# Optimization experiments

Measured on AMD Instinct MI355X. Metric: run time of the kernel, lower is better.

The kernel has to match this reference:

```python
import jax, jax.numpy as jnp
import numpy as np

B, T, H = 1024, 1024, 64


def _lstm_cell(x, h, c, w_ih, w_hh, b_ih, b_hh):
    # gates: [B, 4H] in PyTorch order i, f, g, o
    g = x @ w_ih.T + h @ w_hh.T + b_ih + b_hh
    i, f, gg, o = jnp.split(g, 4, axis=-1)
    i = jax.nn.sigmoid(i)
    f = jax.nn.sigmoid(f)
    gg = jnp.tanh(gg)
    o = jax.nn.sigmoid(o)
    c_new = f * c + i * gg
    h_new = o * jnp.tanh(c_new)
    return h_new, c_new


def setup_inputs() -> dict:
    key = jax.random.key(0)
    ks = jax.random.split(key, 12)
    s = 1.0 / np.sqrt(H)  # torch default init scale
    r = lambda k, shape: jax.random.normal(k, shape, dtype=jnp.float32) * s
    return {
        "x": jax.random.normal(ks[0], (B, T), dtype=jnp.float32),
        "w_ih1": r(ks[1], (4 * H, 1)),
        "w_hh1": r(ks[2], (4 * H, H)),
        "b_ih1": r(ks[3], (4 * H,)),
        "b_hh1": r(ks[4], (4 * H,)),
        "w_ih2": r(ks[5], (4 * H, H)),
        "w_hh2": r(ks[6], (4 * H, H)),
        "b_ih2": r(ks[7], (4 * H,)),
        "b_hh2": r(ks[8], (4 * H,)),
        "w_lin": r(ks[9], (1, H)),
        "b_lin": r(ks[10], (1,)),
        "future_preds": 0,
    }


def reference(x, w_ih1, w_hh1, b_ih1, b_hh1, w_ih2, w_hh2, b_ih2, b_hh2,
              w_lin, b_lin, future_preds):
    bsz = x.shape[0]
    h1 = jnp.zeros((bsz, H), x.dtype)
    c1 = jnp.zeros((bsz, H), x.dtype)
    h2 = jnp.zeros((bsz, H), x.dtype)
    c2 = jnp.zeros((bsz, H), x.dtype)

    def step(carry, x_t):
        h1, c1, h2, c2 = carry
        h1, c1 = _lstm_cell(x_t, h1, c1, w_ih1, w_hh1, b_ih1, b_hh1)
        h2, c2 = _lstm_cell(h1, h2, c2, w_ih2, w_hh2, b_ih2, b_hh2)
        out = h2 @ w_lin.T + b_lin  # [B, 1]
        return (h1, c1, h2, c2), out

    xs = x.T[:, :, None]  # [T, B, 1]
    carry, outs = jax.lax.scan(step, (h1, c1, h2, c2), xs)
    outputs = outs[:, :, 0].T  # [B, T]

    if future_preds > 0:
        last = outs[-1]  # [B, 1]

        def fstep(carry, _):
            h1, c1, h2, c2, prev = carry
            h1, c1 = _lstm_cell(prev, h1, c1, w_ih1, w_hh1, b_ih1, b_hh1)
            h2, c2 = _lstm_cell(h1, h2, c2, w_ih2, w_hh2, b_ih2, b_hh2)
            out = h2 @ w_lin.T + b_lin
            return (h1, c1, h2, c2, out), out

        _, fouts = jax.lax.scan(fstep, (*carry, last), None, length=future_preds)
        outputs = jnp.concatenate([outputs, fouts[:, :, 0].T], axis=1)

    return outputs
```

## Files before the change

### kernel.cpp

```cpp
#include <hip/hip_runtime.h>
#include <hip/hip_bf16.h>


typedef _Float16 f16x8 __attribute__((ext_vector_type(8)));
typedef float    f32x4 __attribute__((ext_vector_type(4)));

namespace {
constexpr int Bb = 1024;
constexpr int Tt = 1024;
constexpr int NBat = 4;
constexpr int HSTR = 80;
constexpr int XSTR = 1025;

__device__ __forceinline__ float sigm_pre(float a) {
    return __builtin_amdgcn_rcpf(1.0f + __builtin_amdgcn_exp2f(a));
}
__device__ __forceinline__ float tanh_pre(float a) {
    return fmaf(2.0f, __builtin_amdgcn_rcpf(1.0f + __builtin_amdgcn_exp2f(a)), -1.0f);
}
__device__ __forceinline__ float tanh_f(float x) {
    float e = __builtin_amdgcn_exp2f(-2.8853900817779268f * x);
    return fmaf(2.0f, __builtin_amdgcn_rcpf(1.0f + e), -1.0f);
}
__device__ __forceinline__ bool detect_f32(const void* w) {
    const unsigned short* p = (const unsigned short*)w;
    int sane = 0;
    for (int i = 0; i < 64; ++i) {
        int e = (p[2 * i] >> 7) & 0xFF;
        if (e >= 107 && e <= 129) ++sane;
    }
    return sane < 32;
}
__device__ __forceinline__ float ld(const void* p, int i, bool f32) {
    return f32 ? ((const float*)p)[i]
               : __bfloat162float(((const __hip_bfloat16*)p)[i]);
}
__device__ __forceinline__ void st(void* p, int i, float v, bool f32) {
    if (f32) ((float*)p)[i] = v;
    else     ((__hip_bfloat16*)p)[i] = __float2bfloat16(v);
}
__device__ __forceinline__ void poll_flags(const int* f, int tp, int tq, int lane) {
    const int idx = lane & 7;
    const int thr = (idx < 4) ? tp : tq;
    for (;;) {
        int v = ((const volatile int*)f)[idx];
        if (__all(v >= thr)) break;
    }
    __builtin_amdgcn_sched_barrier(0);
    asm volatile("" ::: "memory");
}
}

__global__ __launch_bounds__(512, 1) void lstm2_kernel(
    const void* __restrict__ x,
    const void* __restrict__ w_ih1,
    const void* __restrict__ w_hh1,
    const void* __restrict__ b_ih1,
    const void* __restrict__ b_hh1,
    const void* __restrict__ w_ih2,
    const void* __restrict__ w_hh2,
    const void* __restrict__ b_ih2,
    const void* __restrict__ b_hh2,
    const void* __restrict__ w_lin,
    const void* __restrict__ b_lin,
    void* __restrict__ out)
{
    const int tid  = threadIdx.x;
    const int lane = tid & 63;
    const int w    = tid >> 6;
    const int gw   = w & 3;
    const bool isP = w < 4;
    const int m    = lane & 15;
    const int quad = lane >> 4;
    const int bb   = blockIdx.x * NBat;

    const bool f32 = detect_f32(w_hh1);

    __shared__ float                  xs[NBat * XSTR];
    __shared__ __align__(16) _Float16 h1ring[4][NBat * HSTR];
    __shared__ __align__(16) _Float16 h2buf[2][NBat * HSTR];
    __shared__ __align__(16) float    headp[4][NBat][4];
    __shared__ float                  outbuf[NBat * Tt];
    __shared__ int                    flg[8];

    for (int i = tid; i < NBat * 1024; i += 512)
        xs[(i >> 10) * XSTR + (i & 1023)] = ld(x, (bb + (i >> 10)) * Tt + (i & 1023), f32);
    for (int i = tid; i < NBat * HSTR; i += 512) {
        h1ring[0][i] = (_Float16)0; h1ring[1][i] = (_Float16)0;
        h1ring[2][i] = (_Float16)0; h1ring[3][i] = (_Float16)0;
        h2buf[0][i] = (_Float16)0;  h2buf[1][i] = (_Float16)0;
    }
    if (tid < 8) flg[tid] = 0;

    const int arow = lane & 15;
    const int g_ld = arow & 3;
    const int u_ld = arow >> 2;
    const float scA = (g_ld == 2) ? -2.8853900817779268f : -1.4426950408889634f;
    f16x8 wfA[4][2], wfB[4][2];
    {
        const void* MA = isP ? w_hh1 : w_ih2;
#pragma unroll
        for (int q = 0; q < 4; ++q) {
            const int row = 64 * g_ld + 16 * gw + 4 * q + u_ld;
#pragma unroll
            for (int s = 0; s < 2; ++s) {
                const int base = row * 64 + 32 * s + quad * 8;
                if (f32) {
                    const float* A = (const float*)MA;
                    const float* B = (const float*)w_hh2;
#pragma unroll
                    for (int j = 0; j < 8; ++j) {
                        wfA[q][s][j] = (_Float16)(scA * A[base + j]);
                        wfB[q][s][j] = isP ? (_Float16)0.0f
                                           : (_Float16)(scA * B[base + j]);
                    }
                } else {
                    const __hip_bfloat16* A = (const __hip_bfloat16*)MA;
                    const __hip_bfloat16* B = (const __hip_bfloat16*)w_hh2;
#pragma unroll
                    for (int j = 0; j < 8; ++j) {
                        wfA[q][s][j] = (_Float16)(scA * __bfloat162float(A[base + j]));
                        wfB[q][s][j] = isP ? (_Float16)0.0f
                                           : (_Float16)(scA * __bfloat162float(B[base + j]));
                    }
                }
            }
        }
    }
    f32x4 bv[4], wxv[4];
#pragma unroll
    for (int q = 0; q < 4; ++q)
#pragma unroll
        for (int r = 0; r < 4; ++r) {
            const int row = 64 * r + 16 * gw + 4 * q + quad;
            const float sg = (r == 2) ? -2.8853900817779268f : -1.4426950408889634f;
            bv[q][r] = sg * (isP ? (ld(b_ih1, row, f32) + ld(b_hh1, row, f32))
                                 : (ld(b_ih2, row, f32) + ld(b_hh2, row, f32)));
            wxv[q][r] = isP ? sg * ld(w_ih1, row, f32) : 0.0f;
        }
    const int q2   = m >> 2;
    const int bsel = m & 3;
    const int hidx = bsel * HSTR + 16 * gw + 4 * q2 + quad;
    const bool s1 = (q2 & 1) != 0, s2 = (q2 & 2) != 0;
    const float wl_u = ld(w_lin, 16 * gw + 4 * q2 + quad, f32);
    const float blin = ld(b_lin, 0, f32);
    float cst = 0.0f;
    __syncthreads();

    if (isP) {
#pragma unroll 4
        for (int t = 0; t < Tt; ++t) {
            const float xt = xs[bsel * XSTR + t];
            f32x4 ai[4];
#pragma unroll
            for (int q = 0; q < 4; ++q)
#pragma unroll
                for (int r = 0; r < 4; ++r)
                    ai[q][r] = fmaf(xt, wxv[q][r], bv[q][r]);
            poll_flags(flg, t, t - 3, lane);
            f32x4 acc[4];
            if (t > 0) {
                const _Float16* hp = h1ring[(t - 1) & 3] + bsel * HSTR;
                const f16x8 pa0 = *(const f16x8*)(hp + quad * 8);
                const f16x8 pa1 = *(const f16x8*)(hp + 32 + quad * 8);
                __builtin_amdgcn_s_setprio(1);
#pragma unroll
                for (int q = 0; q < 4; ++q) {
                    f32x4 p0 = __builtin_amdgcn_mfma_f32_16x16x32_f16(wfA[q][0], pa0, ai[q], 0, 0, 0);
                    f32x4 p1 = __builtin_amdgcn_mfma_f32_16x16x32_f16(wfA[q][1], pa1, f32x4{0,0,0,0}, 0, 0, 0);
                    acc[q] = p0 + p1;
                }
                __builtin_amdgcn_s_setprio(0);
            } else {
#pragma unroll
                for (int q = 0; q < 4; ++q) acc[q] = ai[q];
            }
            f32x4 g;
#pragma unroll
            for (int r = 0; r < 4; ++r) {
                float lo = s1 ? acc[1][r] : acc[0][r];
                float hi = s1 ? acc[3][r] : acc[2][r];
                g[r] = s2 ? hi : lo;
            }
            float ig = sigm_pre(g[0]), fg = sigm_pre(g[1]);
            float gg = tanh_pre(g[2]), og = sigm_pre(g[3]);
            cst = fmaf(fg, cst, ig * gg);
            h1ring[t & 3][hidx] = (_Float16)(og * tanh_f(cst));
            if (lane == 0) {
                asm volatile("" ::: "memory");
                *(volatile int*)&flg[gw] = t + 1;
            }
        }
    } else {
#pragma unroll 4
        for (int u = 0; u < Tt; ++u) {
            poll_flags(flg, u + 1, u, lane);
            if (u > 1 && w == 4 && lane < NBat) {
                f32x4 v = *(const f32x4*)&headp[(u - 2) & 3][lane][0];
                outbuf[lane * Tt + (u - 2)] = blin + (v[0] + v[1]) + (v[2] + v[3]);
            }
            const _Float16* h1p = h1ring[u & 3] + bsel * HSTR;
            const _Float16* h2p = h2buf[(u + 1) & 1] + bsel * HSTR;
            const f16x8 pa0 = *(const f16x8*)(h1p + quad * 8);
            const f16x8 pa1 = *(const f16x8*)(h1p + 32 + quad * 8);
            const f16x8 pb0 = *(const f16x8*)(h2p + quad * 8);
            const f16x8 pb1 = *(const f16x8*)(h2p + 32 + quad * 8);
            f32x4 acc[4];
            __builtin_amdgcn_s_setprio(1);
#pragma unroll
            for (int q = 0; q < 4; ++q) {
                f32x4 p2 = __builtin_amdgcn_mfma_f32_16x16x32_f16(wfA[q][0], pa0, bv[q], 0, 0, 0);
                p2 = __builtin_amdgcn_mfma_f32_16x16x32_f16(wfA[q][1], pa1, p2, 0, 0, 0);
                f32x4 p3 = __builtin_amdgcn_mfma_f32_16x16x32_f16(wfB[q][0], pb0, f32x4{0,0,0,0}, 0, 0, 0);
                p3 = __builtin_amdgcn_mfma_f32_16x16x32_f16(wfB[q][1], pb1, p3, 0, 0, 0);
                acc[q] = p2 + p3;
            }
            __builtin_amdgcn_s_setprio(0);
            f32x4 g;
#pragma unroll
            for (int r = 0; r < 4; ++r) {
                float lo = s1 ? acc[1][r] : acc[0][r];
                float hi = s1 ? acc[3][r] : acc[2][r];
                g[r] = s2 ? hi : lo;
            }
            float ig = sigm_pre(g[0]), fg = sigm_pre(g[1]);
            float gg = tanh_pre(g[2]), og = sigm_pre(g[3]);
            cst = fmaf(fg, cst, ig * gg);
            float h = og * tanh_f(cst);
            h2buf[u & 1][hidx] = (_Float16)h;
            if (lane == 0) {
                asm volatile("" ::: "memory");
                *(volatile int*)&flg[4 + gw] = u + 1;
            }
            float p = h * wl_u;
            p += __shfl_xor(p, 4);
            p += __shfl_xor(p, 8);
            p += __shfl_xor(p, 16);
            p += __shfl_xor(p, 32);
            if (lane < NBat)
                headp[u & 3][lane][gw] = p;
        }
        if (w == 4) {
            poll_flags(flg, 0, Tt, lane);
            if (lane < NBat) {
                f32x4 v2 = *(const f32x4*)&headp[(Tt - 2) & 3][lane][0];
                outbuf[lane * Tt + (Tt - 2)] = blin + (v2[0] + v2[1]) + (v2[2] + v2[3]);
                f32x4 v1 = *(const f32x4*)&headp[(Tt - 1) & 3][lane][0];
                outbuf[lane * Tt + (Tt - 1)] = blin + (v1[0] + v1[1]) + (v1[2] + v1[3]);
            }
        }
    }
    __syncthreads();
    for (int i = tid; i < NBat * Tt; i += 512)
        st(out, (bb + (i >> 10)) * Tt + (i & 1023), outbuf[i], f32);
}

extern "C" void kernel_launch(void* const* d_in, const int* in_sizes, int n_in,
                              void* d_out, int out_size, void* d_ws, size_t ws_size,
                              hipStream_t stream)
{
    (void)in_sizes; (void)n_in; (void)out_size; (void)d_ws; (void)ws_size;
    lstm2_kernel<<<dim3(Bb / NBat), dim3(512), 0, stream>>>(
        d_in[0], d_in[1], d_in[2], d_in[3], d_in[4], d_in[5],
        d_in[6], d_in[7], d_in[8], d_in[9], d_in[10], d_out);
}
```

Measured before the change: 718.0 us.

## Split block batch into two interleaved groups to overlap recurrent step latency

Splits the four batch rows each block handles into two independent groups of two, each with its own h ring buffers, head partials and sync flags, and interleaves their timestep processing in both the layer-1 and layer-2 wavefronts. The aim is to hide the serial MFMA, activation and flag-poll latency of one group behind the work of the other. In exchange, each group's MFMA uses only 2 of 16 B columns, so half the lanes compute duplicate results that are not stored. It also doubles the number of MFMAs and flag polls per timestep.

Result: slower. 1.295 ms (+80.4%).

```diff
diff --git a/kernel.cpp b/kernel.cpp
--- a/kernel.cpp
+++ b/kernel.cpp
@@ -9,6 +9,8 @@
 constexpr int Bb = 1024;
 constexpr int Tt = 1024;
 constexpr int NBat = 4;
+constexpr int NG   = 2;
+constexpr int GB   = 2;
 constexpr int HSTR = 80;
 constexpr int XSTR = 1025;
 
@@ -77,20 +79,19 @@
     const bool f32 = detect_f32(w_hh1);
 
     __shared__ float                  xs[NBat * XSTR];
-    __shared__ __align__(16) _Float16 h1ring[4][NBat * HSTR];
-    __shared__ __align__(16) _Float16 h2buf[2][NBat * HSTR];
-    __shared__ __align__(16) float    headp[4][NBat][4];
+    __shared__ __align__(16) _Float16 h1ring[NG][4][GB * HSTR];
+    __shared__ __align__(16) _Float16 h2buf[NG][2][GB * HSTR];
+    __shared__ __align__(16) float    headp[NG][4][GB][4];
     __shared__ float                  outbuf[NBat * Tt];
-    __shared__ int                    flg[8];
+    __shared__ int                    flg[NG][8];
 
     for (int i = tid; i < NBat * 1024; i += 512)
         xs[(i >> 10) * XSTR + (i & 1023)] = ld(x, (bb + (i >> 10)) * Tt + (i & 1023), f32);
-    for (int i = tid; i < NBat * HSTR; i += 512) {
-        h1ring[0][i] = (_Float16)0; h1ring[1][i] = (_Float16)0;
-        h1ring[2][i] = (_Float16)0; h1ring[3][i] = (_Float16)0;
-        h2buf[0][i] = (_Float16)0;  h2buf[1][i] = (_Float16)0;
-    }
-    if (tid < 8) flg[tid] = 0;
+    for (int i = tid; i < NG * 4 * GB * HSTR; i += 512)
+        (&h1ring[0][0][0])[i] = (_Float16)0;
+    for (int i = tid; i < NG * 2 * GB * HSTR; i += 512)
+        (&h2buf[0][0][0])[i] = (_Float16)0;
+    if (tid < NG * 8) (&flg[0][0])[tid] = 0;
 
     const int arow = lane & 15;
     const int g_ld = arow & 3;
@@ -138,115 +139,127 @@
                                  : (ld(b_ih2, row, f32) + ld(b_hh2, row, f32)));
             wxv[q][r] = isP ? sg * ld(w_ih1, row, f32) : 0.0f;
         }
-    const int q2   = m >> 2;
-    const int bsel = m & 3;
+    const int bsel = m & 1;
+    const int q2   = (m >> 1) & 3;
+    const bool dup = (m & 8) != 0;
     const int hidx = bsel * HSTR + 16 * gw + 4 * q2 + quad;
-    const bool s1 = (q2 & 1) != 0, s2 = (q2 & 2) != 0;
+    const bool s1 = (m & 2) != 0, s2 = (m & 4) != 0;
     const float wl_u = ld(w_lin, 16 * gw + 4 * q2 + quad, f32);
     const float blin = ld(b_lin, 0, f32);
-    float cst = 0.0f;
+    float csA = 0.0f, csB = 0.0f;
     __syncthreads();
 
     if (isP) {
 #pragma unroll 4
         for (int t = 0; t < Tt; ++t) {
-            const float xt = xs[bsel * XSTR + t];
-            f32x4 ai[4];
-#pragma unroll
-            for (int q = 0; q < 4; ++q)
-#pragma unroll
-                for (int r = 0; r < 4; ++r)
-                    ai[q][r] = fmaf(xt, wxv[q][r], bv[q][r]);
-            poll_flags(flg, t, t - 3, lane);
-            f32x4 acc[4];
-            if (t > 0) {
-                const _Float16* hp = h1ring[(t - 1) & 3] + bsel * HSTR;
-                const f16x8 pa0 = *(const f16x8*)(hp + quad * 8);
-                const f16x8 pa1 = *(const f16x8*)(hp + 32 + quad * 8);
-                __builtin_amdgcn_s_setprio(1);
-#pragma unroll
-                for (int q = 0; q < 4; ++q) {
-                    f32x4 p0 = __builtin_amdgcn_mfma_f32_16x16x32_f16(wfA[q][0], pa0, ai[q], 0, 0, 0);
-                    f32x4 p1 = __builtin_amdgcn_mfma_f32_16x16x32_f16(wfA[q][1], pa1, f32x4{0,0,0,0}, 0, 0, 0);
-                    acc[q] = p0 + p1;
-                }
-                __builtin_amdgcn_s_setprio(0);
-            } else {
-#pragma unroll
-                for (int q = 0; q < 4; ++q) acc[q] = ai[q];
-            }
-            f32x4 g;
-#pragma unroll
-            for (int r = 0; r < 4; ++r) {
-                float lo = s1 ? acc[1][r] : acc[0][r];
-                float hi = s1 ? acc[3][r] : acc[2][r];
-                g[r] = s2 ? hi : lo;
-            }
-            float ig = sigm_pre(g[0]), fg = sigm_pre(g[1]);
-            float gg = tanh_pre(g[2]), og = sigm_pre(g[3]);
-            cst = fmaf(fg, cst, ig * gg);
-            h1ring[t & 3][hidx] = (_Float16)(og * tanh_f(cst));
-            if (lane == 0) {
-                asm volatile("" ::: "memory");
-                *(volatile int*)&flg[gw] = t + 1;
+#pragma unroll
+            for (int g = 0; g < NG; ++g) {
+                float& cs = (g == 0) ? csA : csB;
+                const float xt = xs[(g * GB + bsel) * XSTR + t];
+                f32x4 ai[4];
+#pragma unroll
+                for (int q = 0; q < 4; ++q)
+#pragma unroll
+                    for (int r = 0; r < 4; ++r)
+                        ai[q][r] = fmaf(xt, wxv[q][r], bv[q][r]);
+                poll_flags(&flg[g][0], t, t - 3, lane);
+                f32x4 acc[4];
+                if (t > 0) {
+                    const _Float16* hp = &h1ring[g][(t - 1) & 3][bsel * HSTR];
+                    const f16x8 pa0 = *(const f16x8*)(hp + quad * 8);
+                    const f16x8 pa1 = *(const f16x8*)(hp + 32 + quad * 8);
+                    __builtin_amdgcn_s_setprio(1);
+#pragma unroll
+                    for (int q = 0; q < 4; ++q) {
+                        f32x4 p0 = __builtin_amdgcn_mfma_f32_16x16x32_f16(wfA[q][0], pa0, ai[q], 0, 0, 0);
+                        f32x4 p1 = __builtin_amdgcn_mfma_f32_16x16x32_f16(wfA[q][1], pa1, f32x4{0,0,0,0}, 0, 0, 0);
+                        acc[q] = p0 + p1;
+                    }
+                    __builtin_amdgcn_s_setprio(0);
+                } else {
+#pragma unroll
+                    for (int q = 0; q < 4; ++q) acc[q] = ai[q];
+                }
+                f32x4 gt;
+#pragma unroll
+                for (int r = 0; r < 4; ++r) {
+                    float lo = s1 ? acc[1][r] : acc[0][r];
+                    float hi = s1 ? acc[3][r] : acc[2][r];
+                    gt[r] = s2 ? hi : lo;
+                }
+                float ig = sigm_pre(gt[0]), fg = sigm_pre(gt[1]);
+                float gg = tanh_pre(gt[2]), og = sigm_pre(gt[3]);
+                cs = fmaf(fg, cs, ig * gg);
+                float h = og * tanh_f(cs);
+                if (!dup) h1ring[g][t & 3][hidx] = (_Float16)h;
+                if (lane == 0) {
+                    asm volatile("" ::: "memory");
+                    *(volatile int*)&flg[g][gw] = t + 1;
+                }
             }
         }
     } else {
 #pragma unroll 4
         for (int u = 0; u < Tt; ++u) {
-            poll_flags(flg, u + 1, u, lane);
-            if (u > 1 && w == 4 && lane < NBat) {
-                f32x4 v = *(const f32x4*)&headp[(u - 2) & 3][lane][0];
-                outbuf[lane * Tt + (u - 2)] = blin + (v[0] + v[1]) + (v[2] + v[3]);
-            }
-            const _Float16* h1p = h1ring[u & 3] + bsel * HSTR;
-            const _Float16* h2p = h2buf[(u + 1) & 1] + bsel * HSTR;
-            const f16x8 pa0 = *(const f16x8*)(h1p + quad * 8);
-            const f16x8 pa1 = *(const f16x8*)(h1p + 32 + quad * 8);
-            const f16x8 pb0 = *(const f16x8*)(h2p + quad * 8);
-            const f16x8 pb1 = *(const f16x8*)(h2p + 32 + quad * 8);
-            f32x4 acc[4];
-            __builtin_amdgcn_s_setprio(1);
-#pragma unroll
-            for (int q = 0; q < 4; ++q) {
-                f32x4 p2 = __builtin_amdgcn_mfma_f32_16x16x32_f16(wfA[q][0], pa0, bv[q], 0, 0, 0);
-                p2 = __builtin_amdgcn_mfma_f32_16x16x32_f16(wfA[q][1], pa1, p2, 0, 0, 0);
-                f32x4 p3 = __builtin_amdgcn_mfma_f32_16x16x32_f16(wfB[q][0], pb0, f32x4{0,0,0,0}, 0, 0, 0);
-                p3 = __builtin_amdgcn_mfma_f32_16x16x32_f16(wfB[q][1], pb1, p3, 0, 0, 0);
-                acc[q] = p2 + p3;
-            }
-            __builtin_amdgcn_s_setprio(0);
-            f32x4 g;
-#pragma unroll
-            for (int r = 0; r < 4; ++r) {
-                float lo = s1 ? acc[1][r] : acc[0][r];
-                float hi = s1 ? acc[3][r] : acc[2][r];
-                g[r] = s2 ? hi : lo;
-            }
-            float ig = sigm_pre(g[0]), fg = sigm_pre(g[1]);
-            float gg = tanh_pre(g[2]), og = sigm_pre(g[3]);
-            cst = fmaf(fg, cst, ig * gg);
-            float h = og * tanh_f(cst);
-            h2buf[u & 1][hidx] = (_Float16)h;
-            if (lane == 0) {
-                asm volatile("" ::: "memory");
-                *(volatile int*)&flg[4 + gw] = u + 1;
-            }
-            float p = h * wl_u;
-            p += __shfl_xor(p, 4);
-            p += __shfl_xor(p, 8);
-            p += __shfl_xor(p, 16);
-            p += __shfl_xor(p, 32);
-            if (lane < NBat)
-                headp[u & 3][lane][gw] = p;
+#pragma unroll
+            for (int g = 0; g < NG; ++g) {
+                float& cs = (g == 0) ? csA : csB;
+                poll_flags(&flg[g][0], u + 1, u, lane);
+                if (u > 1 && w == 4 && lane < GB) {
+                    f32x4 v = *(const f32x4*)&headp[g][(u - 2) & 3][lane][0];
+                    outbuf[(g * GB + lane) * Tt + (u - 2)] = blin + (v[0] + v[1]) + (v[2] + v[3]);
+                }
+                const _Float16* h1p = &h1ring[g][u & 3][bsel * HSTR];
+                const _Float16* h2p = &h2buf[g][(u + 1) & 1][bsel * HSTR];
+                const f16x8 pa0 = *(const f16x8*)(h1p + quad * 8);
+                const f16x8 pa1 = *(const f16x8*)(h1p + 32 + quad * 8);
+                const f16x8 pb0 = *(const f16x8*)(h2p + quad * 8);
+                const f16x8 pb1 = *(const f16x8*)(h2p + 32 + quad * 8);
+                f32x4 acc[4];
+                __builtin_amdgcn_s_setprio(1);
+#pragma unroll
+                for (int q = 0; q < 4; ++q) {
+                    f32x4 p2 = __builtin_amdgcn_mfma_f32_16x16x32_f16(wfA[q][0], pa0, bv[q], 0, 0, 0);
+                    p2 = __builtin_amdgcn_mfma_f32_16x16x32_f16(wfA[q][1], pa1, p2, 0, 0, 0);
+                    f32x4 p3 = __builtin_amdgcn_mfma_f32_16x16x32_f16(wfB[q][0], pb0, f32x4{0,0,0,0}, 0, 0, 0);
+                    p3 = __builtin_amdgcn_mfma_f32_16x16x32_f16(wfB[q][1], pb1, p3, 0, 0, 0);
+                    acc[q] = p2 + p3;
+                }
+                __builtin_amdgcn_s_setprio(0);
+                f32x4 gt;
+#pragma unroll
+                for (int r = 0; r < 4; ++r) {
+                    float lo = s1 ? acc[1][r] : acc[0][r];
+                    float hi = s1 ? acc[3][r] : acc[2][r];
+                    gt[r] = s2 ? hi : lo;
+                }
+                float ig = sigm_pre(gt[0]), fg = sigm_pre(gt[1]);
+                float gg = tanh_pre(gt[2]), og = sigm_pre(gt[3]);
+                cs = fmaf(fg, cs, ig * gg);
+                float h = og * tanh_f(cs);
+                if (!dup) h2buf[g][u & 1][hidx] = (_Float16)h;
+                if (lane == 0) {
+                    asm volatile("" ::: "memory");
+                    *(volatile int*)&flg[g][4 + gw] = u + 1;
+                }
+                float p = h * wl_u;
+                p += __shfl_xor(p, 2);
+                p += __shfl_xor(p, 4);
+                p += __shfl_xor(p, 16);
+                p += __shfl_xor(p, 32);
+                if (lane < GB) headp[g][u & 3][lane][gw] = p;
+            }
         }
         if (w == 4) {
-            poll_flags(flg, 0, Tt, lane);
-            if (lane < NBat) {
-                f32x4 v2 = *(const f32x4*)&headp[(Tt - 2) & 3][lane][0];
-                outbuf[lane * Tt + (Tt - 2)] = blin + (v2[0] + v2[1]) + (v2[2] + v2[3]);
-                f32x4 v1 = *(const f32x4*)&headp[(Tt - 1) & 3][lane][0];
-                outbuf[lane * Tt + (Tt - 1)] = blin + (v1[0] + v1[1]) + (v1[2] + v1[3]);
+#pragma unroll
+            for (int g = 0; g < NG; ++g) {
+                poll_flags(&flg[g][0], 0, Tt, lane);
+                if (lane < GB) {
+                    f32x4 v2 = *(const f32x4*)&headp[g][(Tt - 2) & 3][lane][0];
+                    outbuf[(g * GB + lane) * Tt + (Tt - 2)] = blin + (v2[0] + v2[1]) + (v2[2] + v2[3]);
+                    f32x4 v1 = *(const f32x4*)&headp[g][(Tt - 1) & 3][lane][0];
+                    outbuf[(g * GB + lane) * Tt + (Tt - 1)] = blin + (v1[0] + v1[1]) + (v1[2] + v1[3]);
+                }
             }
         }
     }
```

## Merge layer-1 and layer-2 wavefronts into one skewed per-wave pipeline

Applied to the files above, without the earlier changes.

Replaces the producer/consumer split (4 waves for layer 1, 4 for layer 2, 512 threads) with 4 waves that each compute layer 1 at step t and layer 2 at step t-1, using 256 threads per block. Each wave now holds all three weight matrices in registers and only one set of flags is polled per step, with an epilogue for the final layer-2 step. This cuts cross-wave flag handshakes and wave count, at the cost of serializing both layers' MFMA and activation work within a wave and raising register pressure.

Result: slower. 1.038 ms (+44.6%).

```diff
diff --git a/kernel.cpp b/kernel.cpp
--- a/kernel.cpp
+++ b/kernel.cpp
@@ -39,9 +39,8 @@
     if (f32) ((float*)p)[i] = v;
     else     ((__hip_bfloat16*)p)[i] = __float2bfloat16(v);
 }
-__device__ __forceinline__ void poll_flags(const int* f, int tp, int tq, int lane) {
-    const int idx = lane & 7;
-    const int thr = (idx < 4) ? tp : tq;
+__device__ __forceinline__ void poll_flags(const int* f, int thr, int lane) {
+    const int idx = lane & 3;
     for (;;) {
         int v = ((const volatile int*)f)[idx];
         if (__all(v >= thr)) break;
@@ -51,7 +50,7 @@
 }
 }
 
-__global__ __launch_bounds__(512, 1) void lstm2_kernel(
+__global__ __launch_bounds__(256, 1) void lstm2_kernel(
     const void* __restrict__ x,
     const void* __restrict__ w_ih1,
     const void* __restrict__ w_hh1,
@@ -67,9 +66,7 @@
 {
     const int tid  = threadIdx.x;
     const int lane = tid & 63;
-    const int w    = tid >> 6;
-    const int gw   = w & 3;
-    const bool isP = w < 4;
+    const int gw   = tid >> 6;
     const int m    = lane & 15;
     const int quad = lane >> 4;
     const int bb   = blockIdx.x * NBat;
@@ -81,62 +78,61 @@
     __shared__ __align__(16) _Float16 h2buf[2][NBat * HSTR];
     __shared__ __align__(16) float    headp[4][NBat][4];
     __shared__ float                  outbuf[NBat * Tt];
-    __shared__ int                    flg[8];
-
-    for (int i = tid; i < NBat * 1024; i += 512)
+    __shared__ int                    flg[4];
+
+    for (int i = tid; i < NBat * 1024; i += 256)
         xs[(i >> 10) * XSTR + (i & 1023)] = ld(x, (bb + (i >> 10)) * Tt + (i & 1023), f32);
-    for (int i = tid; i < NBat * HSTR; i += 512) {
+    for (int i = tid; i < NBat * HSTR; i += 256) {
         h1ring[0][i] = (_Float16)0; h1ring[1][i] = (_Float16)0;
         h1ring[2][i] = (_Float16)0; h1ring[3][i] = (_Float16)0;
         h2buf[0][i] = (_Float16)0;  h2buf[1][i] = (_Float16)0;
     }
-    if (tid < 8) flg[tid] = 0;
+    if (tid < 4) flg[tid] = 0;
 
     const int arow = lane & 15;
     const int g_ld = arow & 3;
     const int u_ld = arow >> 2;
     const float scA = (g_ld == 2) ? -2.8853900817779268f : -1.4426950408889634f;
-    f16x8 wfA[4][2], wfB[4][2];
-    {
-        const void* MA = isP ? w_hh1 : w_ih2;
-#pragma unroll
-        for (int q = 0; q < 4; ++q) {
-            const int row = 64 * g_ld + 16 * gw + 4 * q + u_ld;
-#pragma unroll
-            for (int s = 0; s < 2; ++s) {
-                const int base = row * 64 + 32 * s + quad * 8;
-                if (f32) {
-                    const float* A = (const float*)MA;
-                    const float* B = (const float*)w_hh2;
-#pragma unroll
-                    for (int j = 0; j < 8; ++j) {
-                        wfA[q][s][j] = (_Float16)(scA * A[base + j]);
-                        wfB[q][s][j] = isP ? (_Float16)0.0f
-                                           : (_Float16)(scA * B[base + j]);
-                    }
-                } else {
-                    const __hip_bfloat16* A = (const __hip_bfloat16*)MA;
-                    const __hip_bfloat16* B = (const __hip_bfloat16*)w_hh2;
-#pragma unroll
-                    for (int j = 0; j < 8; ++j) {
-                        wfA[q][s][j] = (_Float16)(scA * __bfloat162float(A[base + j]));
-                        wfB[q][s][j] = isP ? (_Float16)0.0f
-                                           : (_Float16)(scA * __bfloat162float(B[base + j]));
-                    }
+    f16x8 wf1[4][2], wf2[4][2], wf3[4][2];
+#pragma unroll
+    for (int q = 0; q < 4; ++q) {
+        const int row = 64 * g_ld + 16 * gw + 4 * q + u_ld;
+#pragma unroll
+        for (int s = 0; s < 2; ++s) {
+            const int base = row * 64 + 32 * s + quad * 8;
+            if (f32) {
+                const float* A1 = (const float*)w_hh1;
+                const float* A2 = (const float*)w_ih2;
+                const float* A3 = (const float*)w_hh2;
+#pragma unroll
+                for (int j = 0; j < 8; ++j) {
+                    wf1[q][s][j] = (_Float16)(scA * A1[base + j]);
+                    wf2[q][s][j] = (_Float16)(scA * A2[base + j]);
+                    wf3[q][s][j] = (_Float16)(scA * A3[base + j]);
                 }
-            }
-        }
-    }
-    f32x4 bv[4], wxv[4];
+            } else {
+                const __hip_bfloat16* A1 = (const __hip_bfloat16*)w_hh1;
+                const __hip_bfloat16* A2 = (const __hip_bfloat16*)w_ih2;
+                const __hip_bfloat16* A3 = (const __hip_bfloat16*)w_hh2;
+#pragma unroll
+                for (int j = 0; j < 8; ++j) {
+                    wf1[q][s][j] = (_Float16)(scA * __bfloat162float(A1[base + j]));
+                    wf2[q][s][j] = (_Float16)(scA * __bfloat162float(A2[base + j]));
+                    wf3[q][s][j] = (_Float16)(scA * __bfloat162float(A3[base + j]));
+                }
+            }
+        }
+    }
+    f32x4 bv1[4], bv2[4], wxv[4];
 #pragma unroll
     for (int q = 0; q < 4; ++q)
 #pragma unroll
         for (int r = 0; r < 4; ++r) {
             const int row = 64 * r + 16 * gw + 4 * q + quad;
             const float sg = (r == 2) ? -2.8853900817779268f : -1.4426950408889634f;
-            bv[q][r] = sg * (isP ? (ld(b_ih1, row, f32) + ld(b_hh1, row, f32))
-                                 : (ld(b_ih2, row, f32) + ld(b_hh2, row, f32)));
-            wxv[q][r] = isP ? sg * ld(w_ih1, row, f32) : 0.0f;
+            bv1[q][r] = sg * (ld(b_ih1, row, f32) + ld(b_hh1, row, f32));
+            bv2[q][r] = sg * (ld(b_ih2, row, f32) + ld(b_hh2, row, f32));
+            wxv[q][r] = sg * ld(w_ih1, row, f32);
         }
     const int q2   = m >> 2;
     const int bsel = m & 3;
@@ -144,114 +140,147 @@
     const bool s1 = (q2 & 1) != 0, s2 = (q2 & 2) != 0;
     const float wl_u = ld(w_lin, 16 * gw + 4 * q2 + quad, f32);
     const float blin = ld(b_lin, 0, f32);
-    float cst = 0.0f;
+    float c1 = 0.0f, c2 = 0.0f;
+    f16x8 pa0{}, pa1{};
     __syncthreads();
 
-    if (isP) {
 #pragma unroll 4
-        for (int t = 0; t < Tt; ++t) {
-            const float xt = xs[bsel * XSTR + t];
-            f32x4 ai[4];
-#pragma unroll
-            for (int q = 0; q < 4; ++q)
-#pragma unroll
-                for (int r = 0; r < 4; ++r)
-                    ai[q][r] = fmaf(xt, wxv[q][r], bv[q][r]);
-            poll_flags(flg, t, t - 3, lane);
+    for (int t = 0; t < Tt; ++t) {
+        const float xt = xs[bsel * XSTR + t];
+        f32x4 ai[4];
+#pragma unroll
+        for (int q = 0; q < 4; ++q)
+#pragma unroll
+            for (int r = 0; r < 4; ++r)
+                ai[q][r] = fmaf(xt, wxv[q][r], bv1[q][r]);
+        poll_flags(flg, t, lane);
+        f32x4 g1;
+        if (t > 0) {
+            const _Float16* hp = h1ring[(t - 1) & 3] + bsel * HSTR;
+            pa0 = *(const f16x8*)(hp + quad * 8);
+            pa1 = *(const f16x8*)(hp + 32 + quad * 8);
             f32x4 acc[4];
-            if (t > 0) {
-                const _Float16* hp = h1ring[(t - 1) & 3] + bsel * HSTR;
-                const f16x8 pa0 = *(const f16x8*)(hp + quad * 8);
-                const f16x8 pa1 = *(const f16x8*)(hp + 32 + quad * 8);
-                __builtin_amdgcn_s_setprio(1);
-#pragma unroll
-                for (int q = 0; q < 4; ++q) {
-                    f32x4 p0 = __builtin_amdgcn_mfma_f32_16x16x32_f16(wfA[q][0], pa0, ai[q], 0, 0, 0);
-                    f32x4 p1 = __builtin_amdgcn_mfma_f32_16x16x32_f16(wfA[q][1], pa1, f32x4{0,0,0,0}, 0, 0, 0);
-                    acc[q] = p0 + p1;
-                }
-                __builtin_amdgcn_s_setprio(0);
-            } else {
-#pragma unroll
-                for (int q = 0; q < 4; ++q) acc[q] = ai[q];
-            }
-            f32x4 g;
+            __builtin_amdgcn_s_setprio(1);
+#pragma unroll
+            for (int q = 0; q < 4; ++q) {
+                f32x4 p0 = __builtin_amdgcn_mfma_f32_16x16x32_f16(wf1[q][0], pa0, ai[q], 0, 0, 0);
+                f32x4 p1 = __builtin_amdgcn_mfma_f32_16x16x32_f16(wf1[q][1], pa1, f32x4{0,0,0,0}, 0, 0, 0);
+                acc[q] = p0 + p1;
+            }
+            __builtin_amdgcn_s_setprio(0);
 #pragma unroll
             for (int r = 0; r < 4; ++r) {
                 float lo = s1 ? acc[1][r] : acc[0][r];
                 float hi = s1 ? acc[3][r] : acc[2][r];
-                g[r] = s2 ? hi : lo;
-            }
-            float ig = sigm_pre(g[0]), fg = sigm_pre(g[1]);
-            float gg = tanh_pre(g[2]), og = sigm_pre(g[3]);
-            cst = fmaf(fg, cst, ig * gg);
-            h1ring[t & 3][hidx] = (_Float16)(og * tanh_f(cst));
-            if (lane == 0) {
-                asm volatile("" ::: "memory");
-                *(volatile int*)&flg[gw] = t + 1;
-            }
-        }
-    } else {
-#pragma unroll 4
-        for (int u = 0; u < Tt; ++u) {
-            poll_flags(flg, u + 1, u, lane);
-            if (u > 1 && w == 4 && lane < NBat) {
-                f32x4 v = *(const f32x4*)&headp[(u - 2) & 3][lane][0];
-                outbuf[lane * Tt + (u - 2)] = blin + (v[0] + v[1]) + (v[2] + v[3]);
-            }
-            const _Float16* h1p = h1ring[u & 3] + bsel * HSTR;
-            const _Float16* h2p = h2buf[(u + 1) & 1] + bsel * HSTR;
-            const f16x8 pa0 = *(const f16x8*)(h1p + quad * 8);
-            const f16x8 pa1 = *(const f16x8*)(h1p + 32 + quad * 8);
+                g1[r] = s2 ? hi : lo;
+            }
+        } else {
+#pragma unroll
+            for (int r = 0; r < 4; ++r)
+                g1[r] = s2 ? (s1 ? ai[3][r] : ai[2][r])
+                           : (s1 ? ai[1][r] : ai[0][r]);
+        }
+        {
+            float ig = sigm_pre(g1[0]), fg = sigm_pre(g1[1]);
+            float gg = tanh_pre(g1[2]), og = sigm_pre(g1[3]);
+            c1 = fmaf(fg, c1, ig * gg);
+            h1ring[t & 3][hidx] = (_Float16)(og * tanh_f(c1));
+        }
+        if (t > 0) {
+            const _Float16* h2p = h2buf[t & 1] + bsel * HSTR;
             const f16x8 pb0 = *(const f16x8*)(h2p + quad * 8);
             const f16x8 pb1 = *(const f16x8*)(h2p + 32 + quad * 8);
             f32x4 acc[4];
             __builtin_amdgcn_s_setprio(1);
 #pragma unroll
             for (int q = 0; q < 4; ++q) {
-                f32x4 p2 = __builtin_amdgcn_mfma_f32_16x16x32_f16(wfA[q][0], pa0, bv[q], 0, 0, 0);
-                p2 = __builtin_amdgcn_mfma_f32_16x16x32_f16(wfA[q][1], pa1, p2, 0, 0, 0);
-                f32x4 p3 = __builtin_amdgcn_mfma_f32_16x16x32_f16(wfB[q][0], pb0, f32x4{0,0,0,0}, 0, 0, 0);
-                p3 = __builtin_amdgcn_mfma_f32_16x16x32_f16(wfB[q][1], pb1, p3, 0, 0, 0);
+                f32x4 p2 = __builtin_amdgcn_mfma_f32_16x16x32_f16(wf2[q][0], pa0, bv2[q], 0, 0, 0);
+                p2 = __builtin_amdgcn_mfma_f32_16x16x32_f16(wf2[q][1], pa1, p2, 0, 0, 0);
+                f32x4 p3 = __builtin_amdgcn_mfma_f32_16x16x32_f16(wf3[q][0], pb0, f32x4{0,0,0,0}, 0, 0, 0);
+                p3 = __builtin_amdgcn_mfma_f32_16x16x32_f16(wf3[q][1], pb1, p3, 0, 0, 0);
                 acc[q] = p2 + p3;
             }
             __builtin_amdgcn_s_setprio(0);
-            f32x4 g;
+            f32x4 g2;
 #pragma unroll
             for (int r = 0; r < 4; ++r) {
                 float lo = s1 ? acc[1][r] : acc[0][r];
                 float hi = s1 ? acc[3][r] : acc[2][r];
-                g[r] = s2 ? hi : lo;
-            }
-            float ig = sigm_pre(g[0]), fg = sigm_pre(g[1]);
-            float gg = tanh_pre(g[2]), og = sigm_pre(g[3]);
-            cst = fmaf(fg, cst, ig * gg);
-            float h = og * tanh_f(cst);
-            h2buf[u & 1][hidx] = (_Float16)h;
-            if (lane == 0) {
-                asm volatile("" ::: "memory");
-                *(volatile int*)&flg[4 + gw] = u + 1;
-            }
+                g2[r] = s2 ? hi : lo;
+            }
+            float ig = sigm_pre(g2[0]), fg = sigm_pre(g2[1]);
+            float gg = tanh_pre(g2[2]), og = sigm_pre(g2[3]);
+            c2 = fmaf(fg, c2, ig * gg);
+            float h = og * tanh_f(c2);
+            h2buf[(t - 1) & 1][hidx] = (_Float16)h;
             float p = h * wl_u;
             p += __shfl_xor(p, 4);
             p += __shfl_xor(p, 8);
             p += __shfl_xor(p, 16);
             p += __shfl_xor(p, 32);
             if (lane < NBat)
-                headp[u & 3][lane][gw] = p;
-        }
-        if (w == 4) {
-            poll_flags(flg, 0, Tt, lane);
-            if (lane < NBat) {
-                f32x4 v2 = *(const f32x4*)&headp[(Tt - 2) & 3][lane][0];
-                outbuf[lane * Tt + (Tt - 2)] = blin + (v2[0] + v2[1]) + (v2[2] + v2[3]);
-                f32x4 v1 = *(const f32x4*)&headp[(Tt - 1) & 3][lane][0];
-                outbuf[lane * Tt + (Tt - 1)] = blin + (v1[0] + v1[1]) + (v1[2] + v1[3]);
-            }
+                headp[(t - 1) & 3][lane][gw] = p;
+        }
+        if (t >= 2 && gw == (t & 3) && lane < NBat) {
+            f32x4 v = *(const f32x4*)&headp[(t - 2) & 3][lane][0];
+            outbuf[lane * Tt + (t - 2)] = blin + (v[0] + v[1]) + (v[2] + v[3]);
+        }
+        if (lane == 0) {
+            asm volatile("" ::: "memory");
+            *(volatile int*)&flg[gw] = t + 1;
+        }
+    }
+
+    poll_flags(flg, Tt, lane);
+    {
+        const _Float16* hp = h1ring[(Tt - 1) & 3] + bsel * HSTR;
+        pa0 = *(const f16x8*)(hp + quad * 8);
+        pa1 = *(const f16x8*)(hp + 32 + quad * 8);
+        const _Float16* h2p = h2buf[Tt & 1] + bsel * HSTR;
+        const f16x8 pb0 = *(const f16x8*)(h2p + quad * 8);
+        const f16x8 pb1 = *(const f16x8*)(h2p + 32 + quad * 8);
+        f32x4 acc[4];
+#pragma unroll
+        for (int q = 0; q < 4; ++q) {
+            f32x4 p2 = __builtin_amdgcn_mfma_f32_16x16x32_f16(wf2[q][0], pa0, bv2[q], 0, 0, 0);
+            p2 = __builtin_amdgcn_mfma_f32_16x16x32_f16(wf2[q][1], pa1, p2, 0, 0, 0);
+            f32x4 p3 = __builtin_amdgcn_mfma_f32_16x16x32_f16(wf3[q][0], pb0, f32x4{0,0,0,0}, 0, 0, 0);
+            p3 = __builtin_amdgcn_mfma_f32_16x16x32_f16(wf3[q][1], pb1, p3, 0, 0, 0);
+            acc[q] = p2 + p3;
+        }
+        f32x4 g2;
+#pragma unroll
+        for (int r = 0; r < 4; ++r) {
+            float lo = s1 ? acc[1][r] : acc[0][r];
+            float hi = s1 ? acc[3][r] : acc[2][r];
+            g2[r] = s2 ? hi : lo;
+        }
+        float ig = sigm_pre(g2[0]), fg = sigm_pre(g2[1]);
+        float gg = tanh_pre(g2[2]), og = sigm_pre(g2[3]);
+        c2 = fmaf(fg, c2, ig * gg);
+        float h = og * tanh_f(c2);
+        float p = h * wl_u;
+        p += __shfl_xor(p, 4);
+        p += __shfl_xor(p, 8);
+        p += __shfl_xor(p, 16);
+        p += __shfl_xor(p, 32);
+        if (lane < NBat) headp[(Tt - 1) & 3][lane][gw] = p;
+    }
+    if (lane == 0) {
+        asm volatile("" ::: "memory");
+        *(volatile int*)&flg[gw] = Tt + 1;
+    }
+    if (gw == 0) {
+        poll_flags(flg, Tt + 1, lane);
+        if (lane < NBat) {
+            f32x4 v2 = *(const f32x4*)&headp[(Tt - 2) & 3][lane][0];
+            outbuf[lane * Tt + (Tt - 2)] = blin + (v2[0] + v2[1]) + (v2[2] + v2[3]);
+            f32x4 v1 = *(const f32x4*)&headp[(Tt - 1) & 3][lane][0];
+            outbuf[lane * Tt + (Tt - 1)] = blin + (v1[0] + v1[1]) + (v1[2] + v1[3]);
         }
     }
     __syncthreads();
-    for (int i = tid; i < NBat * Tt; i += 512)
+    for (int i = tid; i < NBat * Tt; i += 256)
         st(out, (bb + (i >> 10)) * Tt + (i & 1023), outbuf[i], f32);
 }
 
@@ -260,7 +289,7 @@
                               hipStream_t stream)
 {
     (void)in_sizes; (void)n_in; (void)out_size; (void)d_ws; (void)ws_size;
-    lstm2_kernel<<<dim3(Bb / NBat), dim3(512), 0, stream>>>(
+    lstm2_kernel<<<dim3(Bb / NBat), dim3(256), 0, stream>>>(
         d_in[0], d_in[1], d_in[2], d_in[3], d_in[4], d_in[5],
         d_in[6], d_in[7], d_in[8], d_in[9], d_in[10], d_out);
 }
```
